# Kernel tuning notes

Measured on AMD Instinct MI355X. Metric: run time of the kernel, lower is better.

## Reference

```python
import jax, jax.numpy as jnp
import numpy as np

B, S, D, H = 16, 8192, 128, 256
N_ITER = 5
LR = 0.1
EPS = 1e-5


def setup_inputs() -> dict:
    key = jax.random.key(0)
    ks = jax.random.split(key, 12)
    sc = 0.02
    return {
        "embeddings": jax.random.normal(ks[0], (B, S, D), dtype=jnp.float32),
        # self_predictor: Linear(D->H), LayerNorm(H), ReLU, Linear(H->D)
        "W1": jax.random.normal(ks[1], (D, H), dtype=jnp.float32) * sc,
        "b1": jnp.zeros((H,), dtype=jnp.float32),
        "ln_g": jnp.ones((H,), dtype=jnp.float32),
        "ln_b": jnp.zeros((H,), dtype=jnp.float32),
        "W2": jax.random.normal(ks[2], (H, D), dtype=jnp.float32) * sc,
        "b2": jnp.zeros((D,), dtype=jnp.float32),
        # context_gate: Linear(2D->H), ReLU, Linear(H->D), Sigmoid
        "Wg1": jax.random.normal(ks[3], (2 * D, H), dtype=jnp.float32) * sc,
        "bg1": jnp.zeros((H,), dtype=jnp.float32),
        "Wg2": jax.random.normal(ks[4], (H, D), dtype=jnp.float32) * sc,
        "bg2": jnp.zeros((D,), dtype=jnp.float32),
    }


def _layernorm(x, g, b):
    mu = jnp.mean(x, axis=-1, keepdims=True)
    var = jnp.var(x, axis=-1, keepdims=True)
    return (x - mu) * jax.lax.rsqrt(var + EPS) * g + b


def _context(refined):
    # neighbor-average context; edges use their single neighbor (seq_len > 1)
    interior = 0.5 * (refined[:, :-2] + refined[:, 2:])        # [B, S-2, D]
    first = refined[:, 1:2]                                    # [B, 1, D]
    last = refined[:, -2:-1]                                   # [B, 1, D]
    return jnp.concatenate([first, interior, last], axis=1)    # [B, S, D]


def reference(embeddings, W1, b1, ln_g, ln_b, W2, b2, Wg1, bg1, Wg2, bg2):
    refined = embeddings
    for _ in range(N_ITER):
        # self-predictor (dropout=0 / eval)
        h = jax.nn.relu(_layernorm(refined @ W1 + b1, ln_g, ln_b))  # [B,S,H]
        predicted = h @ W2 + b2                                     # [B,S,D]
        error = embeddings - predicted
        # batched context gate over all positions at once
        gate_in = jnp.concatenate([refined, _context(refined)], axis=-1)  # [B,S,2D]
        gate = jax.nn.sigmoid(jax.nn.relu(gate_in @ Wg1 + bg1) @ Wg2 + bg2)
        refined = refined + LR * gate * error
    return refined
```

## Files before the change

kernel.cpp:

```cpp
#include <hip/hip_runtime.h>

#define BB   16
#define SS   8192
#define DD   128
#define HH   256
#define NTOK (BB * SS)
#define TM   64
#define THREADS 256
#define LRATE 0.1f
#define EPSV  1e-5f
#define XCST 264
#define HST  264

typedef short  bfrag __attribute__((ext_vector_type(8)));
typedef float  f32x4 __attribute__((ext_vector_type(4)));
typedef unsigned short u16;

__device__ __forceinline__ u16 f2bf(float x) {
    unsigned u = __float_as_uint(x);
    unsigned r = (u + 0x7FFFu + ((u >> 16) & 1u)) >> 16;
    return (u16)r;
}

__global__ void prep_weights(const float* __restrict__ W1, const float* __restrict__ W2,
                             const float* __restrict__ Wg1, const float* __restrict__ Wg2,
                             u16* __restrict__ wsw) {
    int i = blockIdx.x * 256 + threadIdx.x;
    if (i < 32768) { int n = i >> 7, k = i & 127; wsw[i] = f2bf(W1[k * 256 + n]); return; }
    i -= 32768;
    if (i < 32768) { int n = i >> 8, k = i & 255; wsw[32768 + n * 256 + k] = f2bf(W2[k * 128 + n]); return; }
    i -= 32768;
    if (i < 65536) { int n = i >> 8, k = i & 255; wsw[65536 + n * 256 + k] = f2bf(Wg1[k * 256 + n]); return; }
    i -= 65536;
    { int n = i >> 8, k = i & 255; wsw[131072 + n * 256 + k] = f2bf(Wg2[k * 128 + n]); }
}

__global__ __launch_bounds__(THREADS, 2)
void refine_iter(const float* __restrict__ cur, const float* __restrict__ emb,
                 float* __restrict__ outp,
                 const u16* __restrict__ w1t, const u16* __restrict__ w2t,
                 const u16* __restrict__ wg1t, const u16* __restrict__ wg2t,
                 const float* __restrict__ b1, const float* __restrict__ lng,
                 const float* __restrict__ lnb, const float* __restrict__ b2,
                 const float* __restrict__ bg1, const float* __restrict__ bg2)
{
    __shared__ __align__(16) u16 XC[TM][XCST];
    __shared__ __align__(16) u16 Hb[TM][HST];
    __shared__ float red1[TM][4];
    __shared__ float red2[TM][4];

    const int t    = threadIdx.x;
    const int g0   = blockIdx.x * TM;
    const int lane = t & 63;
    const int wid  = t >> 6;
    const int l16  = lane & 15;
    const int lk8  = (lane >> 4) * 8;
    const int l4   = (lane >> 4) * 4;

    #pragma unroll
    for (int k = 0; k < 8; ++k) {
        const int f = t + k * THREADS;
        const int m = f >> 5;
        const int o = (f & 31) * 4;
        const int gt = g0 + m;
        const int s  = gt & (SS - 1);
        const int rowbase = gt - s;
        const int sp = (s == 0) ? 1 : s - 1;
        const int sn = (s == SS - 1) ? (SS - 2) : s + 1;
        const float4 xv = *(const float4*)(cur + (size_t)gt * DD + o);
        const float4 av = *(const float4*)(cur + (size_t)(rowbase + sp) * DD + o);
        const float4 bv = *(const float4*)(cur + (size_t)(rowbase + sn) * DD + o);
        ushort4 xu; xu.x = f2bf(xv.x); xu.y = f2bf(xv.y); xu.z = f2bf(xv.z); xu.w = f2bf(xv.w);
        *(ushort4*)&XC[m][o] = xu;
        ushort4 cu;
        cu.x = f2bf(0.5f * (av.x + bv.x)); cu.y = f2bf(0.5f * (av.y + bv.y));
        cu.z = f2bf(0.5f * (av.z + bv.z)); cu.w = f2bf(0.5f * (av.w + bv.w));
        *(ushort4*)&XC[m][128 + o] = cu;
    }

    float emb_pre[4][2][4];
    {
        const int n0b = wid * 32;
        #pragma unroll
        for (int rt = 0; rt < 4; ++rt)
            #pragma unroll
            for (int ct = 0; ct < 2; ++ct)
                #pragma unroll
                for (int r = 0; r < 4; ++r)
                    emb_pre[rt][ct][r] = emb[(size_t)(g0 + rt * 16 + l4 + r) * DD + n0b + ct * 16 + l16];
    }
    __syncthreads();

    const f32x4 zf = {0.f, 0.f, 0.f, 0.f};
    float mu[4][4], rs[4][4];

    {
        const int n0 = wid * 64;
        f32x4 acc[4][4];
        #pragma unroll
        for (int rt = 0; rt < 4; ++rt)
            #pragma unroll
            for (int ct = 0; ct < 4; ++ct) acc[rt][ct] = zf;
        #pragma unroll
        for (int h = 0; h < 2; ++h) {
            bfrag wb[8];
            #pragma unroll
            for (int i = 0; i < 2; ++i)
                #pragma unroll
                for (int ks = 0; ks < 4; ++ks)
                    wb[i * 4 + ks] = *(const bfrag*)(w1t + (size_t)(n0 + (h * 2 + i) * 16 + l16) * 128 + ks * 32 + lk8);
            __builtin_amdgcn_sched_barrier(0);
            #pragma unroll
            for (int ks = 0; ks < 4; ++ks) {
                bfrag af[4];
                #pragma unroll
                for (int rt = 0; rt < 4; ++rt)
                    af[rt] = *(const bfrag*)&XC[rt * 16 + l16][ks * 32 + lk8];
                #pragma unroll
                for (int i = 0; i < 2; ++i)
                    #pragma unroll
                    for (int rt = 0; rt < 4; ++rt)
                        acc[rt][h * 2 + i] = __builtin_amdgcn_mfma_f32_16x16x32_bf16(af[rt], wb[i * 4 + ks], acc[rt][h * 2 + i], 0, 0, 0);
            }
        }
        #pragma unroll
        for (int ct = 0; ct < 4; ++ct) {
            const float bb = b1[n0 + ct * 16 + l16];
            #pragma unroll
            for (int rt = 0; rt < 4; ++rt)
                #pragma unroll
                for (int r = 0; r < 4; ++r) acc[rt][ct][r] += bb;
        }

        #pragma unroll
        for (int rt = 0; rt < 4; ++rt)
            #pragma unroll
            for (int r = 0; r < 4; ++r) {
                float a = 0.f, q = 0.f;
                #pragma unroll
                for (int ct = 0; ct < 4; ++ct) {
                    const float v = acc[rt][ct][r];
                    a += v; q += v * v;
                }
                #pragma unroll
                for (int m = 1; m <= 8; m <<= 1) {
                    a += __shfl_xor(a, m);
                    q += __shfl_xor(q, m);
                }
                if (l16 == 0) {
                    red1[rt * 16 + l4 + r][wid] = a;
                    red2[rt * 16 + l4 + r][wid] = q;
                }
            }
        __syncthreads();
        #pragma unroll
        for (int rt = 0; rt < 4; ++rt)
            #pragma unroll
            for (int r = 0; r < 4; ++r) {
                const int row = rt * 16 + l4 + r;
                const float4 s1v = *(const float4*)&red1[row][0];
                const float4 s2v = *(const float4*)&red2[row][0];
                const float s1 = s1v.x + s1v.y + s1v.z + s1v.w;
                const float s2 = s2v.x + s2v.y + s2v.z + s2v.w;
                const float m_ = s1 * (1.f / (float)HH);
                mu[rt][r] = m_;
                rs[rt][r] = rsqrtf(s2 * (1.f / (float)HH) - m_ * m_ + EPSV);
            }

        #pragma unroll
        for (int ct = 0; ct < 4; ++ct) {
            const int col = n0 + ct * 16 + l16;
            const float g = lng[col];
            const float b = lnb[col];
            #pragma unroll
            for (int rt = 0; rt < 4; ++rt)
                #pragma unroll
                for (int r = 0; r < 4; ++r) {
                    const float h = fmaxf((acc[rt][ct][r] - mu[rt][r]) * rs[rt][r] * g + b, 0.f);
                    Hb[rt * 16 + l4 + r][col] = f2bf(h);
                }
        }
    }
    __syncthreads();

    float errv[4][2][4];
    {
        const int n0 = wid * 32;
        f32x4 acc[4][2];
        #pragma unroll
        for (int rt = 0; rt < 4; ++rt) { acc[rt][0] = zf; acc[rt][1] = zf; }
        bfrag wb[16];
        #pragma unroll
        for (int ct = 0; ct < 2; ++ct)
            #pragma unroll
            for (int ks = 0; ks < 8; ++ks)
                wb[ct * 8 + ks] = *(const bfrag*)(w2t + (size_t)(n0 + ct * 16 + l16) * 256 + ks * 32 + lk8);
        __builtin_amdgcn_sched_barrier(0);
        #pragma unroll
        for (int ks = 0; ks < 8; ++ks) {
            bfrag af[4];
            #pragma unroll
            for (int rt = 0; rt < 4; ++rt)
                af[rt] = *(const bfrag*)&Hb[rt * 16 + l16][ks * 32 + lk8];
            #pragma unroll
            for (int ct = 0; ct < 2; ++ct)
                #pragma unroll
                for (int rt = 0; rt < 4; ++rt)
                    acc[rt][ct] = __builtin_amdgcn_mfma_f32_16x16x32_bf16(af[rt], wb[ct * 8 + ks], acc[rt][ct], 0, 0, 0);
        }
        #pragma unroll
        for (int ct = 0; ct < 2; ++ct) {
            const float bb = b2[n0 + ct * 16 + l16];
            #pragma unroll
            for (int rt = 0; rt < 4; ++rt)
                #pragma unroll
                for (int r = 0; r < 4; ++r)
                    errv[rt][ct][r] = emb_pre[rt][ct][r] - (acc[rt][ct][r] + bb);
        }
    }

    {
        const int n0 = wid * 64;
        f32x4 acc[4][4];
        #pragma unroll
        for (int rt = 0; rt < 4; ++rt)
            #pragma unroll
            for (int ct = 0; ct < 4; ++ct) acc[rt][ct] = zf;
        #pragma unroll
        for (int h = 0; h < 2; ++h) {
            bfrag wb[16];
            #pragma unroll
            for (int i = 0; i < 2; ++i)
                #pragma unroll
                for (int ks = 0; ks < 8; ++ks)
                    wb[i * 8 + ks] = *(const bfrag*)(wg1t + (size_t)(n0 + (h * 2 + i) * 16 + l16) * 256 + ks * 32 + lk8);
            __builtin_amdgcn_sched_barrier(0);
            #pragma unroll
            for (int ks = 0; ks < 8; ++ks) {
                bfrag af[4];
                #pragma unroll
                for (int rt = 0; rt < 4; ++rt)
                    af[rt] = *(const bfrag*)&XC[rt * 16 + l16][ks * 32 + lk8];
                #pragma unroll
                for (int i = 0; i < 2; ++i)
                    #pragma unroll
                    for (int rt = 0; rt < 4; ++rt)
                        acc[rt][h * 2 + i] = __builtin_amdgcn_mfma_f32_16x16x32_bf16(af[rt], wb[i * 8 + ks], acc[rt][h * 2 + i], 0, 0, 0);
            }
        }
        __syncthreads();
        #pragma unroll
        for (int ct = 0; ct < 4; ++ct) {
            const float bb = bg1[n0 + ct * 16 + l16];
            #pragma unroll
            for (int rt = 0; rt < 4; ++rt)
                #pragma unroll
                for (int r = 0; r < 4; ++r)
                    Hb[rt * 16 + l4 + r][n0 + ct * 16 + l16] = f2bf(fmaxf(acc[rt][ct][r] + bb, 0.f));
        }
    }
    __syncthreads();

    {
        const int n0 = wid * 32;
        f32x4 acc[4][2];
        #pragma unroll
        for (int rt = 0; rt < 4; ++rt) { acc[rt][0] = zf; acc[rt][1] = zf; }
        bfrag wb[16];
        #pragma unroll
        for (int ct = 0; ct < 2; ++ct)
            #pragma unroll
            for (int ks = 0; ks < 8; ++ks)
                wb[ct * 8 + ks] = *(const bfrag*)(wg2t + (size_t)(n0 + ct * 16 + l16) * 256 + ks * 32 + lk8);
        __builtin_amdgcn_sched_barrier(0);
        #pragma unroll
        for (int ks = 0; ks < 8; ++ks) {
            bfrag af[4];
            #pragma unroll
            for (int rt = 0; rt < 4; ++rt)
                af[rt] = *(const bfrag*)&Hb[rt * 16 + l16][ks * 32 + lk8];
            #pragma unroll
            for (int ct = 0; ct < 2; ++ct)
                #pragma unroll
                for (int rt = 0; rt < 4; ++rt)
                    acc[rt][ct] = __builtin_amdgcn_mfma_f32_16x16x32_bf16(af[rt], wb[ct * 8 + ks], acc[rt][ct], 0, 0, 0);
        }
        #pragma unroll
        for (int ct = 0; ct < 2; ++ct) {
            const float bb = bg2[n0 + ct * 16 + l16];
            #pragma unroll
            for (int rt = 0; rt < 4; ++rt)
                #pragma unroll
                for (int r = 0; r < 4; ++r) {
                    const int row = g0 + rt * 16 + l4 + r;
                    const int col = n0 + ct * 16 + l16;
                    const float z = acc[rt][ct][r] + bb;
                    const float gate = 1.f / (1.f + __expf(-z));
                    const float x = cur[(size_t)row * DD + col];
                    outp[(size_t)row * DD + col] = x + LRATE * gate * errv[rt][ct][r];
                }
        }
    }
}

extern "C" void kernel_launch(void* const* d_in, const int* in_sizes, int n_in,
                              void* d_out, int out_size, void* d_ws, size_t ws_size,
                              hipStream_t stream) {
    const float* emb = (const float*)d_in[0];
    const float* W1  = (const float*)d_in[1];
    const float* b1  = (const float*)d_in[2];
    const float* lng = (const float*)d_in[3];
    const float* lnb = (const float*)d_in[4];
    const float* W2  = (const float*)d_in[5];
    const float* b2  = (const float*)d_in[6];
    const float* Wg1 = (const float*)d_in[7];
    const float* bg1 = (const float*)d_in[8];
    const float* Wg2 = (const float*)d_in[9];
    const float* bg2 = (const float*)d_in[10];
    float* out = (float*)d_out;

    u16*   wsw  = (u16*)d_ws;
    float* ping = (float*)((char*)d_ws + (1 << 20));

    const u16* w1t  = wsw;
    const u16* w2t  = wsw + 32768;
    const u16* wg1t = wsw + 65536;
    const u16* wg2t = wsw + 131072;

    prep_weights<<<640, 256, 0, stream>>>(W1, W2, Wg1, Wg2, wsw);

    const dim3 grid(NTOK / TM);
    const dim3 block(THREADS);
    refine_iter<<<grid, block, 0, stream>>>(emb,  emb, out,  w1t, w2t, wg1t, wg2t, b1, lng, lnb, b2, bg1, bg2);
    refine_iter<<<grid, block, 0, stream>>>(out,  emb, ping, w1t, w2t, wg1t, wg2t, b1, lng, lnb, b2, bg1, bg2);
    refine_iter<<<grid, block, 0, stream>>>(ping, emb, out,  w1t, w2t, wg1t, wg2t, b1, lng, lnb, b2, bg1, bg2);
    refine_iter<<<grid, block, 0, stream>>>(out,  emb, ping, w1t, w2t, wg1t, wg2t, b1, lng, lnb, b2, bg1, bg2);
    refine_iter<<<grid, block, 0, stream>>>(ping, emb, out,  w1t, w2t, wg1t, wg2t, b1, lng, lnb, b2, bg1, bg2);
}
```

Measured before the change: 626.9 us.

## Split each 64-token tile across 8 waves instead of 4

Doubles the threads per block to 512 (8 waves), so each wave computes half as many output columns per GEMM stage, and raises the occupancy hint in launch_bounds. The LayerNorm cross-wave reduction now sums 8 partials. Embedding and current-state prefetches move closer to their use. Float-to-bf16 packing switches to the paired hardware conversion intrinsic. The aim is more latency hiding and less register pressure per wave, at the cost of each wave reusing fewer loaded A fragments per MFMA and reloading the same LDS A tiles across more waves.

Measured after the change: 680.5 us. 8.6% more time.

```diff
diff --git a/kernel.cpp b/kernel.cpp
--- a/kernel.cpp
+++ b/kernel.cpp
@@ -1,4 +1,5 @@
 #include <hip/hip_runtime.h>
+#include <hip/hip_bf16.h>
 
 #define BB   16
 #define SS   8192
@@ -6,7 +7,8 @@
 #define HH   256
 #define NTOK (BB * SS)
 #define TM   64
-#define THREADS 256
+#define THREADS 512
+#define NW   8
 #define LRATE 0.1f
 #define EPSV  1e-5f
 #define XCST 264
@@ -20,6 +22,11 @@
     unsigned u = __float_as_uint(x);
     unsigned r = (u + 0x7FFFu + ((u >> 16) & 1u)) >> 16;
     return (u16)r;
+}
+
+__device__ __forceinline__ unsigned pkbf(float lo, float hi) {
+    __hip_bfloat162 h2 = __float22bfloat162_rn(make_float2(lo, hi));
+    unsigned u; __builtin_memcpy(&u, &h2, 4); return u;
 }
 
 __global__ void prep_weights(const float* __restrict__ W1, const float* __restrict__ W2,
@@ -35,7 +42,7 @@
     { int n = i >> 8, k = i & 255; wsw[131072 + n * 256 + k] = f2bf(Wg2[k * 128 + n]); }
 }
 
-__global__ __launch_bounds__(THREADS, 2)
+__global__ __launch_bounds__(THREADS, 4)
 void refine_iter(const float* __restrict__ cur, const float* __restrict__ emb,
                  float* __restrict__ outp,
                  const u16* __restrict__ w1t, const u16* __restrict__ w2t,
@@ -46,8 +53,8 @@
 {
     __shared__ __align__(16) u16 XC[TM][XCST];
     __shared__ __align__(16) u16 Hb[TM][HST];
-    __shared__ float red1[TM][4];
-    __shared__ float red2[TM][4];
+    __shared__ float red1[TM][NW];
+    __shared__ float red2[TM][NW];
 
     const int t    = threadIdx.x;
     const int g0   = blockIdx.x * TM;
@@ -56,9 +63,11 @@
     const int l16  = lane & 15;
     const int lk8  = (lane >> 4) * 8;
     const int l4   = (lane >> 4) * 4;
+    const int nAC  = wid * 32;
+    const int nBD  = wid * 16;
 
     #pragma unroll
-    for (int k = 0; k < 8; ++k) {
+    for (int k = 0; k < 4; ++k) {
         const int f = t + k * THREADS;
         const int m = f >> 5;
         const int o = (f & 31) * 4;
@@ -70,24 +79,12 @@
         const float4 xv = *(const float4*)(cur + (size_t)gt * DD + o);
         const float4 av = *(const float4*)(cur + (size_t)(rowbase + sp) * DD + o);
         const float4 bv = *(const float4*)(cur + (size_t)(rowbase + sn) * DD + o);
-        ushort4 xu; xu.x = f2bf(xv.x); xu.y = f2bf(xv.y); xu.z = f2bf(xv.z); xu.w = f2bf(xv.w);
-        *(ushort4*)&XC[m][o] = xu;
-        ushort4 cu;
-        cu.x = f2bf(0.5f * (av.x + bv.x)); cu.y = f2bf(0.5f * (av.y + bv.y));
-        cu.z = f2bf(0.5f * (av.z + bv.z)); cu.w = f2bf(0.5f * (av.w + bv.w));
-        *(ushort4*)&XC[m][128 + o] = cu;
-    }
-
-    float emb_pre[4][2][4];
-    {
-        const int n0b = wid * 32;
-        #pragma unroll
-        for (int rt = 0; rt < 4; ++rt)
-            #pragma unroll
-            for (int ct = 0; ct < 2; ++ct)
-                #pragma unroll
-                for (int r = 0; r < 4; ++r)
-                    emb_pre[rt][ct][r] = emb[(size_t)(g0 + rt * 16 + l4 + r) * DD + n0b + ct * 16 + l16];
+        uint2 xq; xq.x = pkbf(xv.x, xv.y); xq.y = pkbf(xv.z, xv.w);
+        *(uint2*)&XC[m][o] = xq;
+        uint2 cq;
+        cq.x = pkbf(0.5f * (av.x + bv.x), 0.5f * (av.y + bv.y));
+        cq.y = pkbf(0.5f * (av.z + bv.z), 0.5f * (av.w + bv.w));
+        *(uint2*)&XC[m][128 + o] = cq;
     }
     __syncthreads();
 
@@ -95,37 +92,31 @@
     float mu[4][4], rs[4][4];
 
     {
-        const int n0 = wid * 64;
-        f32x4 acc[4][4];
-        #pragma unroll
-        for (int rt = 0; rt < 4; ++rt)
-            #pragma unroll
-            for (int ct = 0; ct < 4; ++ct) acc[rt][ct] = zf;
-        #pragma unroll
-        for (int h = 0; h < 2; ++h) {
-            bfrag wb[8];
-            #pragma unroll
-            for (int i = 0; i < 2; ++i)
-                #pragma unroll
-                for (int ks = 0; ks < 4; ++ks)
-                    wb[i * 4 + ks] = *(const bfrag*)(w1t + (size_t)(n0 + (h * 2 + i) * 16 + l16) * 128 + ks * 32 + lk8);
-            __builtin_amdgcn_sched_barrier(0);
-            #pragma unroll
-            for (int ks = 0; ks < 4; ++ks) {
-                bfrag af[4];
+        f32x4 acc[4][2];
+        #pragma unroll
+        for (int rt = 0; rt < 4; ++rt) { acc[rt][0] = zf; acc[rt][1] = zf; }
+        bfrag wb[8];
+        #pragma unroll
+        for (int ct = 0; ct < 2; ++ct)
+            #pragma unroll
+            for (int ks = 0; ks < 4; ++ks)
+                wb[ct * 4 + ks] = *(const bfrag*)(w1t + (size_t)(nAC + ct * 16 + l16) * 128 + ks * 32 + lk8);
+        __builtin_amdgcn_sched_barrier(0);
+        #pragma unroll
+        for (int ks = 0; ks < 4; ++ks) {
+            bfrag af[4];
+            #pragma unroll
+            for (int rt = 0; rt < 4; ++rt)
+                af[rt] = *(const bfrag*)&XC[rt * 16 + l16][ks * 32 + lk8];
+            #pragma unroll
+            for (int ct = 0; ct < 2; ++ct)
                 #pragma unroll
                 for (int rt = 0; rt < 4; ++rt)
-                    af[rt] = *(const bfrag*)&XC[rt * 16 + l16][ks * 32 + lk8];
-                #pragma unroll
-                for (int i = 0; i < 2; ++i)
-                    #pragma unroll
-                    for (int rt = 0; rt < 4; ++rt)
-                        acc[rt][h * 2 + i] = __builtin_amdgcn_mfma_f32_16x16x32_bf16(af[rt], wb[i * 4 + ks], acc[rt][h * 2 + i], 0, 0, 0);
-            }
-        }
-        #pragma unroll
-        for (int ct = 0; ct < 4; ++ct) {
-            const float bb = b1[n0 + ct * 16 + l16];
+                    acc[rt][ct] = __builtin_amdgcn_mfma_f32_16x16x32_bf16(af[rt], wb[ct * 4 + ks], acc[rt][ct], 0, 0, 0);
+        }
+        #pragma unroll
+        for (int ct = 0; ct < 2; ++ct) {
+            const float bb = b1[nAC + ct * 16 + l16];
             #pragma unroll
             for (int rt = 0; rt < 4; ++rt)
                 #pragma unroll
@@ -136,12 +127,9 @@
         for (int rt = 0; rt < 4; ++rt)
             #pragma unroll
             for (int r = 0; r < 4; ++r) {
-                float a = 0.f, q = 0.f;
-                #pragma unroll
-                for (int ct = 0; ct < 4; ++ct) {
-                    const float v = acc[rt][ct][r];
-                    a += v; q += v * v;
-                }
+                const float v0 = acc[rt][0][r], v1 = acc[rt][1][r];
+                float a = v0 + v1;
+                float q = v0 * v0 + v1 * v1;
                 #pragma unroll
                 for (int m = 1; m <= 8; m <<= 1) {
                     a += __shfl_xor(a, m);
@@ -158,43 +146,47 @@
             #pragma unroll
             for (int r = 0; r < 4; ++r) {
                 const int row = rt * 16 + l4 + r;
-                const float4 s1v = *(const float4*)&red1[row][0];
-                const float4 s2v = *(const float4*)&red2[row][0];
-                const float s1 = s1v.x + s1v.y + s1v.z + s1v.w;
-                const float s2 = s2v.x + s2v.y + s2v.z + s2v.w;
+                const float4 a0 = *(const float4*)&red1[row][0];
+                const float4 a1 = *(const float4*)&red1[row][4];
+                const float4 q0 = *(const float4*)&red2[row][0];
+                const float4 q1 = *(const float4*)&red2[row][4];
+                const float s1 = a0.x + a0.y + a0.z + a0.w + a1.x + a1.y + a1.z + a1.w;
+                const float s2 = q0.x + q0.y + q0.z + q0.w + q1.x + q1.y + q1.z + q1.w;
                 const float m_ = s1 * (1.f / (float)HH);
                 mu[rt][r] = m_;
                 rs[rt][r] = rsqrtf(s2 * (1.f / (float)HH) - m_ * m_ + EPSV);
             }
 
-        #pragma unroll
-        for (int ct = 0; ct < 4; ++ct) {
-            const int col = n0 + ct * 16 + l16;
-            const float g = lng[col];
-            const float b = lnb[col];
-            #pragma unroll
-            for (int rt = 0; rt < 4; ++rt)
-                #pragma unroll
-                for (int r = 0; r < 4; ++r) {
-                    const float h = fmaxf((acc[rt][ct][r] - mu[rt][r]) * rs[rt][r] * g + b, 0.f);
-                    Hb[rt * 16 + l4 + r][col] = f2bf(h);
-                }
-        }
+        const float ga = lng[nAC + l16],      ba = lnb[nAC + l16];
+        const float gb = lng[nAC + 16 + l16], bb2 = lnb[nAC + 16 + l16];
+        #pragma unroll
+        for (int rt = 0; rt < 4; ++rt)
+            #pragma unroll
+            for (int r = 0; r < 4; ++r) {
+                const float h0 = fmaxf((acc[rt][0][r] - mu[rt][r]) * rs[rt][r] * ga + ba, 0.f);
+                const float h1 = fmaxf((acc[rt][1][r] - mu[rt][r]) * rs[rt][r] * gb + bb2, 0.f);
+                const unsigned p = pkbf(h0, h1);
+                Hb[rt * 16 + l4 + r][nAC + l16]      = (u16)(p & 0xffffu);
+                Hb[rt * 16 + l4 + r][nAC + 16 + l16] = (u16)(p >> 16);
+            }
     }
     __syncthreads();
 
-    float errv[4][2][4];
+    float errv[4][4];
     {
-        const int n0 = wid * 32;
-        f32x4 acc[4][2];
-        #pragma unroll
-        for (int rt = 0; rt < 4; ++rt) { acc[rt][0] = zf; acc[rt][1] = zf; }
-        bfrag wb[16];
-        #pragma unroll
-        for (int ct = 0; ct < 2; ++ct)
-            #pragma unroll
-            for (int ks = 0; ks < 8; ++ks)
-                wb[ct * 8 + ks] = *(const bfrag*)(w2t + (size_t)(n0 + ct * 16 + l16) * 256 + ks * 32 + lk8);
+        float ep[4][4];
+        #pragma unroll
+        for (int rt = 0; rt < 4; ++rt)
+            #pragma unroll
+            for (int r = 0; r < 4; ++r)
+                ep[rt][r] = emb[(size_t)(g0 + rt * 16 + l4 + r) * DD + nBD + l16];
+        f32x4 acc[4];
+        #pragma unroll
+        for (int rt = 0; rt < 4; ++rt) acc[rt] = zf;
+        bfrag wb[8];
+        #pragma unroll
+        for (int ks = 0; ks < 8; ++ks)
+            wb[ks] = *(const bfrag*)(w2t + (size_t)(nBD + l16) * 256 + ks * 32 + lk8);
         __builtin_amdgcn_sched_barrier(0);
         #pragma unroll
         for (int ks = 0; ks < 8; ++ks) {
@@ -203,75 +195,74 @@
             for (int rt = 0; rt < 4; ++rt)
                 af[rt] = *(const bfrag*)&Hb[rt * 16 + l16][ks * 32 + lk8];
             #pragma unroll
+            for (int rt = 0; rt < 4; ++rt)
+                acc[rt] = __builtin_amdgcn_mfma_f32_16x16x32_bf16(af[rt], wb[ks], acc[rt], 0, 0, 0);
+        }
+        const float bb = b2[nBD + l16];
+        #pragma unroll
+        for (int rt = 0; rt < 4; ++rt)
+            #pragma unroll
+            for (int r = 0; r < 4; ++r)
+                errv[rt][r] = ep[rt][r] - (acc[rt][r] + bb);
+    }
+
+    {
+        f32x4 acc[4][2];
+        #pragma unroll
+        for (int rt = 0; rt < 4; ++rt) { acc[rt][0] = zf; acc[rt][1] = zf; }
+        #pragma unroll
+        for (int h = 0; h < 2; ++h) {
+            bfrag wb[8];
+            #pragma unroll
             for (int ct = 0; ct < 2; ++ct)
                 #pragma unroll
-                for (int rt = 0; rt < 4; ++rt)
-                    acc[rt][ct] = __builtin_amdgcn_mfma_f32_16x16x32_bf16(af[rt], wb[ct * 8 + ks], acc[rt][ct], 0, 0, 0);
-        }
-        #pragma unroll
-        for (int ct = 0; ct < 2; ++ct) {
-            const float bb = b2[n0 + ct * 16 + l16];
-            #pragma unroll
-            for (int rt = 0; rt < 4; ++rt)
-                #pragma unroll
-                for (int r = 0; r < 4; ++r)
-                    errv[rt][ct][r] = emb_pre[rt][ct][r] - (acc[rt][ct][r] + bb);
-        }
-    }
-
-    {
-        const int n0 = wid * 64;
-        f32x4 acc[4][4];
-        #pragma unroll
-        for (int rt = 0; rt < 4; ++rt)
-            #pragma unroll
-            for (int ct = 0; ct < 4; ++ct) acc[rt][ct] = zf;
-        #pragma unroll
-        for (int h = 0; h < 2; ++h) {
-            bfrag wb[16];
-            #pragma unroll
-            for (int i = 0; i < 2; ++i)
-                #pragma unroll
-                for (int ks = 0; ks < 8; ++ks)
-                    wb[i * 8 + ks] = *(const bfrag*)(wg1t + (size_t)(n0 + (h * 2 + i) * 16 + l16) * 256 + ks * 32 + lk8);
+                for (int ks2 = 0; ks2 < 4; ++ks2)
+                    wb[ct * 4 + ks2] = *(const bfrag*)(wg1t + (size_t)(nAC + ct * 16 + l16) * 256 + (h * 4 + ks2) * 32 + lk8);
             __builtin_amdgcn_sched_barrier(0);
             #pragma unroll
-            for (int ks = 0; ks < 8; ++ks) {
+            for (int ks2 = 0; ks2 < 4; ++ks2) {
+                const int ks = h * 4 + ks2;
                 bfrag af[4];
                 #pragma unroll
                 for (int rt = 0; rt < 4; ++rt)
                     af[rt] = *(const bfrag*)&XC[rt * 16 + l16][ks * 32 + lk8];
                 #pragma unroll
-                for (int i = 0; i < 2; ++i)
+                for (int ct = 0; ct < 2; ++ct)
                     #pragma unroll
                     for (int rt = 0; rt < 4; ++rt)
-                        acc[rt][h * 2 + i] = __builtin_amdgcn_mfma_f32_16x16x32_bf16(af[rt], wb[i * 8 + ks], acc[rt][h * 2 + i], 0, 0, 0);
+                        acc[rt][ct] = __builtin_amdgcn_mfma_f32_16x16x32_bf16(af[rt], wb[ct * 4 + ks2], acc[rt][ct], 0, 0, 0);
             }
         }
         __syncthreads();
-        #pragma unroll
-        for (int ct = 0; ct < 4; ++ct) {
-            const float bb = bg1[n0 + ct * 16 + l16];
-            #pragma unroll
-            for (int rt = 0; rt < 4; ++rt)
-                #pragma unroll
-                for (int r = 0; r < 4; ++r)
-                    Hb[rt * 16 + l4 + r][n0 + ct * 16 + l16] = f2bf(fmaxf(acc[rt][ct][r] + bb, 0.f));
-        }
+        const float bga = bg1[nAC + l16];
+        const float bgb = bg1[nAC + 16 + l16];
+        #pragma unroll
+        for (int rt = 0; rt < 4; ++rt)
+            #pragma unroll
+            for (int r = 0; r < 4; ++r) {
+                const float r0v = fmaxf(acc[rt][0][r] + bga, 0.f);
+                const float r1v = fmaxf(acc[rt][1][r] + bgb, 0.f);
+                const unsigned p = pkbf(r0v, r1v);
+                Hb[rt * 16 + l4 + r][nAC + l16]      = (u16)(p & 0xffffu);
+                Hb[rt * 16 + l4 + r][nAC + 16 + l16] = (u16)(p >> 16);
+            }
     }
     __syncthreads();
 
     {
-        const int n0 = wid * 32;
-        f32x4 acc[4][2];
-        #pragma unroll
-        for (int rt = 0; rt < 4; ++rt) { acc[rt][0] = zf; acc[rt][1] = zf; }
-        bfrag wb[16];
-        #pragma unroll
-        for (int ct = 0; ct < 2; ++ct)
-            #pragma unroll
-            for (int ks = 0; ks < 8; ++ks)
-                wb[ct * 8 + ks] = *(const bfrag*)(wg2t + (size_t)(n0 + ct * 16 + l16) * 256 + ks * 32 + lk8);
+        float cp[4][4];
+        #pragma unroll
+        for (int rt = 0; rt < 4; ++rt)
+            #pragma unroll
+            for (int r = 0; r < 4; ++r)
+                cp[rt][r] = cur[(size_t)(g0 + rt * 16 + l4 + r) * DD + nBD + l16];
+        f32x4 acc[4];
+        #pragma unroll
+        for (int rt = 0; rt < 4; ++rt) acc[rt] = zf;
+        bfrag wb[8];
+        #pragma unroll
+        for (int ks = 0; ks < 8; ++ks)
+            wb[ks] = *(const bfrag*)(wg2t + (size_t)(nBD + l16) * 256 + ks * 32 + lk8);
         __builtin_amdgcn_sched_barrier(0);
         #pragma unroll
         for (int ks = 0; ks < 8; ++ks) {
@@ -280,26 +271,18 @@
             for (int rt = 0; rt < 4; ++rt)
                 af[rt] = *(const bfrag*)&Hb[rt * 16 + l16][ks * 32 + lk8];
             #pragma unroll
-            for (int ct = 0; ct < 2; ++ct)
-                #pragma unroll
-                for (int rt = 0; rt < 4; ++rt)
-                    acc[rt][ct] = __builtin_amdgcn_mfma_f32_16x16x32_bf16(af[rt], wb[ct * 8 + ks], acc[rt][ct], 0, 0, 0);
-        }
-        #pragma unroll
-        for (int ct = 0; ct < 2; ++ct) {
-            const float bb = bg2[n0 + ct * 16 + l16];
-            #pragma unroll
-            for (int rt = 0; rt < 4; ++rt)
-                #pragma unroll
-                for (int r = 0; r < 4; ++r) {
-                    const int row = g0 + rt * 16 + l4 + r;
-                    const int col = n0 + ct * 16 + l16;
-                    const float z = acc[rt][ct][r] + bb;
-                    const float gate = 1.f / (1.f + __expf(-z));
-                    const float x = cur[(size_t)row * DD + col];
-                    outp[(size_t)row * DD + col] = x + LRATE * gate * errv[rt][ct][r];
-                }
-        }
+            for (int rt = 0; rt < 4; ++rt)
+                acc[rt] = __builtin_amdgcn_mfma_f32_16x16x32_bf16(af[rt], wb[ks], acc[rt], 0, 0, 0);
+        }
+        const float bb = bg2[nBD + l16];
+        #pragma unroll
+        for (int rt = 0; rt < 4; ++rt)
+            #pragma unroll
+            for (int r = 0; r < 4; ++r) {
+                const float z = acc[rt][r] + bb;
+                const float gate = 1.f / (1.f + __expf(-z));
+                outp[(size_t)(g0 + rt * 16 + l4 + r) * DD + nBD + l16] = cp[rt][r] + LRATE * gate * errv[rt][r];
+            }
     }
 }
 
```

## Prefetch next-stage weight fragments into registers ahead of each GEMM stage

Applied to the files above, without the earlier changes.

Restructures the fused per-tile kernel so each GEMM's weight fragments are loaded into registers one stage early. W2 loads during LayerNorm, Wg1 during the W2 GEMM, and Wg2 plus the residual `cur` values before the last GEMM. Global-load latency is meant to hide behind MFMA and epilogue work instead of stalling at each stage start. It also switches bf16 conversion to packed intrinsics and moves the embedding prefetch earlier. The extra live register arrays raise register pressure, which risks spills or lower occupancy under the two-blocks-per-CU launch bound.

Measured after the change: 719.0 us. +14.7%, slower.

```diff
diff --git a/kernel.cpp b/kernel.cpp
--- a/kernel.cpp
+++ b/kernel.cpp
@@ -1,4 +1,5 @@
 #include <hip/hip_runtime.h>
+#include <hip/hip_bf16.h>
 
 #define BB   16
 #define SS   8192
@@ -20,6 +21,11 @@
     unsigned u = __float_as_uint(x);
     unsigned r = (u + 0x7FFFu + ((u >> 16) & 1u)) >> 16;
     return (u16)r;
+}
+
+__device__ __forceinline__ unsigned pkbf(float lo, float hi) {
+    __hip_bfloat162 h2 = __float22bfloat162_rn(make_float2(lo, hi));
+    unsigned u; __builtin_memcpy(&u, &h2, 4); return u;
 }
 
 __global__ void prep_weights(const float* __restrict__ W1, const float* __restrict__ W2,
@@ -56,6 +62,17 @@
     const int l16  = lane & 15;
     const int lk8  = (lane >> 4) * 8;
     const int l4   = (lane >> 4) * 4;
+    const int nAC  = wid * 64;
+    const int nBD  = wid * 32;
+
+    float ep[4][2][4];
+    #pragma unroll
+    for (int rt = 0; rt < 4; ++rt)
+        #pragma unroll
+        for (int ct = 0; ct < 2; ++ct)
+            #pragma unroll
+            for (int r = 0; r < 4; ++r)
+                ep[rt][ct][r] = emb[(size_t)(g0 + rt * 16 + l4 + r) * DD + nBD + ct * 16 + l16];
 
     #pragma unroll
     for (int k = 0; k < 8; ++k) {
@@ -70,62 +87,57 @@
         const float4 xv = *(const float4*)(cur + (size_t)gt * DD + o);
         const float4 av = *(const float4*)(cur + (size_t)(rowbase + sp) * DD + o);
         const float4 bv = *(const float4*)(cur + (size_t)(rowbase + sn) * DD + o);
-        ushort4 xu; xu.x = f2bf(xv.x); xu.y = f2bf(xv.y); xu.z = f2bf(xv.z); xu.w = f2bf(xv.w);
-        *(ushort4*)&XC[m][o] = xu;
-        ushort4 cu;
-        cu.x = f2bf(0.5f * (av.x + bv.x)); cu.y = f2bf(0.5f * (av.y + bv.y));
-        cu.z = f2bf(0.5f * (av.z + bv.z)); cu.w = f2bf(0.5f * (av.w + bv.w));
-        *(ushort4*)&XC[m][128 + o] = cu;
+        uint2 xq; xq.x = pkbf(xv.x, xv.y); xq.y = pkbf(xv.z, xv.w);
+        *(uint2*)&XC[m][o] = xq;
+        uint2 cq;
+        cq.x = pkbf(0.5f * (av.x + bv.x), 0.5f * (av.y + bv.y));
+        cq.y = pkbf(0.5f * (av.z + bv.z), 0.5f * (av.w + bv.w));
+        *(uint2*)&XC[m][128 + o] = cq;
     }
 
-    float emb_pre[4][2][4];
-    {
-        const int n0b = wid * 32;
-        #pragma unroll
-        for (int rt = 0; rt < 4; ++rt)
-            #pragma unroll
-            for (int ct = 0; ct < 2; ++ct)
-                #pragma unroll
-                for (int r = 0; r < 4; ++r)
-                    emb_pre[rt][ct][r] = emb[(size_t)(g0 + rt * 16 + l4 + r) * DD + n0b + ct * 16 + l16];
-    }
+    bfrag wA[16];
+    #pragma unroll
+    for (int ct = 0; ct < 4; ++ct)
+        #pragma unroll
+        for (int ks = 0; ks < 4; ++ks)
+            wA[ct * 4 + ks] = *(const bfrag*)(w1t + (size_t)(nAC + ct * 16 + l16) * 128 + ks * 32 + lk8);
+    __builtin_amdgcn_sched_barrier(0);
     __syncthreads();
 
     const f32x4 zf = {0.f, 0.f, 0.f, 0.f};
     float mu[4][4], rs[4][4];
 
     {
-        const int n0 = wid * 64;
         f32x4 acc[4][4];
         #pragma unroll
         for (int rt = 0; rt < 4; ++rt)
             #pragma unroll
             for (int ct = 0; ct < 4; ++ct) acc[rt][ct] = zf;
         #pragma unroll
-        for (int h = 0; h < 2; ++h) {
-            bfrag wb[8];
-            #pragma unroll
-            for (int i = 0; i < 2; ++i)
-                #pragma unroll
-                for (int ks = 0; ks < 4; ++ks)
-                    wb[i * 4 + ks] = *(const bfrag*)(w1t + (size_t)(n0 + (h * 2 + i) * 16 + l16) * 128 + ks * 32 + lk8);
-            __builtin_amdgcn_sched_barrier(0);
-            #pragma unroll
-            for (int ks = 0; ks < 4; ++ks) {
-                bfrag af[4];
-                #pragma unroll
-                for (int rt = 0; rt < 4; ++rt)
-                    af[rt] = *(const bfrag*)&XC[rt * 16 + l16][ks * 32 + lk8];
-                #pragma unroll
-                for (int i = 0; i < 2; ++i)
-                    #pragma unroll
-                    for (int rt = 0; rt < 4; ++rt)
-                        acc[rt][h * 2 + i] = __builtin_amdgcn_mfma_f32_16x16x32_bf16(af[rt], wb[i * 4 + ks], acc[rt][h * 2 + i], 0, 0, 0);
-            }
-        }
+        for (int ks = 0; ks < 4; ++ks) {
+            bfrag af[4];
+            #pragma unroll
+            for (int rt = 0; rt < 4; ++rt)
+                af[rt] = *(const bfrag*)&XC[rt * 16 + l16][ks * 32 + lk8];
+            #pragma unroll
+            for (int ct = 0; ct < 4; ++ct)
+                #pragma unroll
+                for (int rt = 0; rt < 4; ++rt)
+                    acc[rt][ct] = __builtin_amdgcn_mfma_f32_16x16x32_bf16(af[rt], wA[ct * 4 + ks], acc[rt][ct], 0, 0, 0);
+        }
+        __builtin_amdgcn_sched_barrier(0);
+
+        bfrag wB[16];
+        #pragma unroll
+        for (int ct = 0; ct < 2; ++ct)
+            #pragma unroll
+            for (int ks = 0; ks < 8; ++ks)
+                wB[ct * 8 + ks] = *(const bfrag*)(w2t + (size_t)(nBD + ct * 16 + l16) * 256 + ks * 32 + lk8);
+        __builtin_amdgcn_sched_barrier(0);
+
         #pragma unroll
         for (int ct = 0; ct < 4; ++ct) {
-            const float bb = b1[n0 + ct * 16 + l16];
+            const float bb = b1[nAC + ct * 16 + l16];
             #pragma unroll
             for (int rt = 0; rt < 4; ++rt)
                 #pragma unroll
@@ -168,137 +180,154 @@
             }
 
         #pragma unroll
-        for (int ct = 0; ct < 4; ++ct) {
-            const int col = n0 + ct * 16 + l16;
-            const float g = lng[col];
-            const float b = lnb[col];
+        for (int cp2 = 0; cp2 < 2; ++cp2) {
+            const float g0v = lng[nAC + (2 * cp2) * 16 + l16],     b0v = lnb[nAC + (2 * cp2) * 16 + l16];
+            const float g1v = lng[nAC + (2 * cp2 + 1) * 16 + l16], b1v = lnb[nAC + (2 * cp2 + 1) * 16 + l16];
             #pragma unroll
             for (int rt = 0; rt < 4; ++rt)
                 #pragma unroll
                 for (int r = 0; r < 4; ++r) {
-                    const float h = fmaxf((acc[rt][ct][r] - mu[rt][r]) * rs[rt][r] * g + b, 0.f);
-                    Hb[rt * 16 + l4 + r][col] = f2bf(h);
+                    const float h0 = fmaxf((acc[rt][2 * cp2][r]     - mu[rt][r]) * rs[rt][r] * g0v + b0v, 0.f);
+                    const float h1 = fmaxf((acc[rt][2 * cp2 + 1][r] - mu[rt][r]) * rs[rt][r] * g1v + b1v, 0.f);
+                    const unsigned p = pkbf(h0, h1);
+                    Hb[rt * 16 + l4 + r][nAC + (2 * cp2) * 16 + l16]     = (u16)(p & 0xffffu);
+                    Hb[rt * 16 + l4 + r][nAC + (2 * cp2 + 1) * 16 + l16] = (u16)(p >> 16);
                 }
         }
-    }
-    __syncthreads();
-
-    float errv[4][2][4];
-    {
-        const int n0 = wid * 32;
-        f32x4 acc[4][2];
-        #pragma unroll
-        for (int rt = 0; rt < 4; ++rt) { acc[rt][0] = zf; acc[rt][1] = zf; }
-        bfrag wb[16];
+        __syncthreads();
+
+        bfrag wC0[16];
         #pragma unroll
         for (int ct = 0; ct < 2; ++ct)
             #pragma unroll
             for (int ks = 0; ks < 8; ++ks)
-                wb[ct * 8 + ks] = *(const bfrag*)(w2t + (size_t)(n0 + ct * 16 + l16) * 256 + ks * 32 + lk8);
+                wC0[ct * 8 + ks] = *(const bfrag*)(wg1t + (size_t)(nAC + ct * 16 + l16) * 256 + ks * 32 + lk8);
         __builtin_amdgcn_sched_barrier(0);
-        #pragma unroll
-        for (int ks = 0; ks < 8; ++ks) {
-            bfrag af[4];
-            #pragma unroll
-            for (int rt = 0; rt < 4; ++rt)
-                af[rt] = *(const bfrag*)&Hb[rt * 16 + l16][ks * 32 + lk8];
-            #pragma unroll
-            for (int ct = 0; ct < 2; ++ct)
-                #pragma unroll
-                for (int rt = 0; rt < 4; ++rt)
-                    acc[rt][ct] = __builtin_amdgcn_mfma_f32_16x16x32_bf16(af[rt], wb[ct * 8 + ks], acc[rt][ct], 0, 0, 0);
-        }
-        #pragma unroll
-        for (int ct = 0; ct < 2; ++ct) {
-            const float bb = b2[n0 + ct * 16 + l16];
-            #pragma unroll
-            for (int rt = 0; rt < 4; ++rt)
-                #pragma unroll
-                for (int r = 0; r < 4; ++r)
-                    errv[rt][ct][r] = emb_pre[rt][ct][r] - (acc[rt][ct][r] + bb);
-        }
-    }
-
-    {
-        const int n0 = wid * 64;
-        f32x4 acc[4][4];
-        #pragma unroll
-        for (int rt = 0; rt < 4; ++rt)
-            #pragma unroll
-            for (int ct = 0; ct < 4; ++ct) acc[rt][ct] = zf;
-        #pragma unroll
-        for (int h = 0; h < 2; ++h) {
-            bfrag wb[16];
-            #pragma unroll
-            for (int i = 0; i < 2; ++i)
-                #pragma unroll
-                for (int ks = 0; ks < 8; ++ks)
-                    wb[i * 8 + ks] = *(const bfrag*)(wg1t + (size_t)(n0 + (h * 2 + i) * 16 + l16) * 256 + ks * 32 + lk8);
-            __builtin_amdgcn_sched_barrier(0);
+
+        float errv[4][2][4];
+        {
+            f32x4 accB[4][2];
+            #pragma unroll
+            for (int rt = 0; rt < 4; ++rt) { accB[rt][0] = zf; accB[rt][1] = zf; }
             #pragma unroll
             for (int ks = 0; ks < 8; ++ks) {
                 bfrag af[4];
                 #pragma unroll
                 for (int rt = 0; rt < 4; ++rt)
+                    af[rt] = *(const bfrag*)&Hb[rt * 16 + l16][ks * 32 + lk8];
+                #pragma unroll
+                for (int ct = 0; ct < 2; ++ct)
+                    #pragma unroll
+                    for (int rt = 0; rt < 4; ++rt)
+                        accB[rt][ct] = __builtin_amdgcn_mfma_f32_16x16x32_bf16(af[rt], wB[ct * 8 + ks], accB[rt][ct], 0, 0, 0);
+            }
+            __builtin_amdgcn_sched_barrier(0);
+            #pragma unroll
+            for (int ct = 0; ct < 2; ++ct) {
+                const float bb = b2[nBD + ct * 16 + l16];
+                #pragma unroll
+                for (int rt = 0; rt < 4; ++rt)
+                    #pragma unroll
+                    for (int r = 0; r < 4; ++r)
+                        errv[rt][ct][r] = ep[rt][ct][r] - (accB[rt][ct][r] + bb);
+            }
+        }
+
+        {
+            bfrag wC1[16];
+            #pragma unroll
+            for (int ct = 0; ct < 2; ++ct)
+                #pragma unroll
+                for (int ks = 0; ks < 8; ++ks)
+                    wC1[ct * 8 + ks] = *(const bfrag*)(wg1t + (size_t)(nAC + (2 + ct) * 16 + l16) * 256 + ks * 32 + lk8);
+            __builtin_amdgcn_sched_barrier(0);
+
+            f32x4 accC[4][4];
+            #pragma unroll
+            for (int rt = 0; rt < 4; ++rt)
+                #pragma unroll
+                for (int ct = 0; ct < 4; ++ct) accC[rt][ct] = zf;
+            #pragma unroll
+            for (int ks = 0; ks < 8; ++ks) {
+                bfrag af[4];
+                #pragma unroll
+                for (int rt = 0; rt < 4; ++rt)
                     af[rt] = *(const bfrag*)&XC[rt * 16 + l16][ks * 32 + lk8];
                 #pragma unroll
-                for (int i = 0; i < 2; ++i)
+                for (int ct = 0; ct < 2; ++ct)
                     #pragma unroll
                     for (int rt = 0; rt < 4; ++rt)
-                        acc[rt][h * 2 + i] = __builtin_amdgcn_mfma_f32_16x16x32_bf16(af[rt], wb[i * 8 + ks], acc[rt][h * 2 + i], 0, 0, 0);
+                        accC[rt][ct] = __builtin_amdgcn_mfma_f32_16x16x32_bf16(af[rt], wC0[ct * 8 + ks], accC[rt][ct], 0, 0, 0);
+                #pragma unroll
+                for (int ct = 0; ct < 2; ++ct)
+                    #pragma unroll
+                    for (int rt = 0; rt < 4; ++rt)
+                        accC[rt][2 + ct] = __builtin_amdgcn_mfma_f32_16x16x32_bf16(af[rt], wC1[ct * 8 + ks], accC[rt][2 + ct], 0, 0, 0);
+            }
+            __syncthreads();
+            #pragma unroll
+            for (int cp2 = 0; cp2 < 2; ++cp2) {
+                const float bga = bg1[nAC + (2 * cp2) * 16 + l16];
+                const float bgb = bg1[nAC + (2 * cp2 + 1) * 16 + l16];
+                #pragma unroll
+                for (int rt = 0; rt < 4; ++rt)
+                    #pragma unroll
+                    for (int r = 0; r < 4; ++r) {
+                        const float r0v = fmaxf(accC[rt][2 * cp2][r]     + bga, 0.f);
+                        const float r1v = fmaxf(accC[rt][2 * cp2 + 1][r] + bgb, 0.f);
+                        const unsigned p = pkbf(r0v, r1v);
+                        Hb[rt * 16 + l4 + r][nAC + (2 * cp2) * 16 + l16]     = (u16)(p & 0xffffu);
+                        Hb[rt * 16 + l4 + r][nAC + (2 * cp2 + 1) * 16 + l16] = (u16)(p >> 16);
+                    }
             }
         }
         __syncthreads();
-        #pragma unroll
-        for (int ct = 0; ct < 4; ++ct) {
-            const float bb = bg1[n0 + ct * 16 + l16];
-            #pragma unroll
-            for (int rt = 0; rt < 4; ++rt)
-                #pragma unroll
-                for (int r = 0; r < 4; ++r)
-                    Hb[rt * 16 + l4 + r][n0 + ct * 16 + l16] = f2bf(fmaxf(acc[rt][ct][r] + bb, 0.f));
-        }
-    }
-    __syncthreads();
-
-    {
-        const int n0 = wid * 32;
-        f32x4 acc[4][2];
-        #pragma unroll
-        for (int rt = 0; rt < 4; ++rt) { acc[rt][0] = zf; acc[rt][1] = zf; }
-        bfrag wb[16];
-        #pragma unroll
-        for (int ct = 0; ct < 2; ++ct)
-            #pragma unroll
-            for (int ks = 0; ks < 8; ++ks)
-                wb[ct * 8 + ks] = *(const bfrag*)(wg2t + (size_t)(n0 + ct * 16 + l16) * 256 + ks * 32 + lk8);
-        __builtin_amdgcn_sched_barrier(0);
-        #pragma unroll
-        for (int ks = 0; ks < 8; ++ks) {
-            bfrag af[4];
-            #pragma unroll
-            for (int rt = 0; rt < 4; ++rt)
-                af[rt] = *(const bfrag*)&Hb[rt * 16 + l16][ks * 32 + lk8];
+
+        {
+            bfrag wD[16];
             #pragma unroll
             for (int ct = 0; ct < 2; ++ct)
                 #pragma unroll
-                for (int rt = 0; rt < 4; ++rt)
-                    acc[rt][ct] = __builtin_amdgcn_mfma_f32_16x16x32_bf16(af[rt], wb[ct * 8 + ks], acc[rt][ct], 0, 0, 0);
-        }
-        #pragma unroll
-        for (int ct = 0; ct < 2; ++ct) {
-            const float bb = bg2[n0 + ct * 16 + l16];
-            #pragma unroll
-            for (int rt = 0; rt < 4; ++rt)
-                #pragma unroll
-                for (int r = 0; r < 4; ++r) {
-                    const int row = g0 + rt * 16 + l4 + r;
-                    const int col = n0 + ct * 16 + l16;
-                    const float z = acc[rt][ct][r] + bb;
-                    const float gate = 1.f / (1.f + __expf(-z));
-                    const float x = cur[(size_t)row * DD + col];
-                    outp[(size_t)row * DD + col] = x + LRATE * gate * errv[rt][ct][r];
-                }
+                for (int ks = 0; ks < 8; ++ks)
+                    wD[ct * 8 + ks] = *(const bfrag*)(wg2t + (size_t)(nBD + ct * 16 + l16) * 256 + ks * 32 + lk8);
+            float cp[4][2][4];
+            #pragma unroll
+            for (int rt = 0; rt < 4; ++rt)
+                #pragma unroll
+                for (int ct = 0; ct < 2; ++ct)
+                    #pragma unroll
+                    for (int r = 0; r < 4; ++r)
+                        cp[rt][ct][r] = cur[(size_t)(g0 + rt * 16 + l4 + r) * DD + nBD + ct * 16 + l16];
+            __builtin_amdgcn_sched_barrier(0);
+
+            f32x4 accD[4][2];
+            #pragma unroll
+            for (int rt = 0; rt < 4; ++rt) { accD[rt][0] = zf; accD[rt][1] = zf; }
+            #pragma unroll
+            for (int ks = 0; ks < 8; ++ks) {
+                bfrag af[4];
+                #pragma unroll
+                for (int rt = 0; rt < 4; ++rt)
+                    af[rt] = *(const bfrag*)&Hb[rt * 16 + l16][ks * 32 + lk8];
+                #pragma unroll
+                for (int ct = 0; ct < 2; ++ct)
+                    #pragma unroll
+                    for (int rt = 0; rt < 4; ++rt)
+                        accD[rt][ct] = __builtin_amdgcn_mfma_f32_16x16x32_bf16(af[rt], wD[ct * 8 + ks], accD[rt][ct], 0, 0, 0);
+            }
+            #pragma unroll
+            for (int ct = 0; ct < 2; ++ct) {
+                const float bb = bg2[nBD + ct * 16 + l16];
+                #pragma unroll
+                for (int rt = 0; rt < 4; ++rt)
+                    #pragma unroll
+                    for (int r = 0; r < 4; ++r) {
+                        const float z = accD[rt][ct][r] + bb;
+                        const float gate = 1.f / (1.f + __expf(-z));
+                        outp[(size_t)(g0 + rt * 16 + l4 + r) * DD + nBD + ct * 16 + l16] =
+                            cp[rt][ct][r] + LRATE * gate * errv[rt][ct][r];
+                    }
+            }
         }
     }
 }
```
